# Kernel tuning notes

Hardware: AMD Instinct MI355X
Metric: run time of the kernel (lower is better)

## Reference

```python
import jax, jax.numpy as jnp
import numpy as np

N = 4096  # number of image features; must equal D because forward does attn @ img_feats.T
D = 4096


def setup_inputs() -> dict:
    key = jax.random.key(0)
    img_feats = jax.random.normal(key, (N, D), dtype=jnp.float32)
    return {"img_feats": img_feats}


def reference(img_feats):
    d = img_feats.shape[-1]
    x = img_feats / jnp.sqrt(jnp.asarray(d, img_feats.dtype))
    sims = x @ x.T  # [N, N] self-similarity
    n = sims.shape[0]
    idx = jnp.arange(n)
    sims = sims.at[idx, idx].set(-jnp.inf)  # mask self-similarity on the diagonal
    attn = jax.nn.softmax(sims, axis=-1)  # [N, N]
    return attn @ x.T  # [N, N] (requires N == D, as in the original)
```

## Files before the change

### kernel.cpp

```cpp
#include <hip/hip_runtime.h>
#include <hip/hip_bf16.h>
#include <stdint.h>

#define N 4096
#define BM 128
#define BN 128
#define BK 64
#define BK8 128

typedef __hip_bfloat16 bf16;
typedef __attribute__((ext_vector_type(8))) __bf16 bfrag;
typedef __attribute__((ext_vector_type(4))) float floatx4;
typedef __attribute__((ext_vector_type(8))) int i32x8;
typedef __attribute__((ext_vector_type(4))) int i32x4;

__device__ __forceinline__ void gld_lds16(const void* g, void* l) {
    __builtin_amdgcn_global_load_lds(
        (const __attribute__((address_space(1))) void*)g,
        (__attribute__((address_space(3))) void*)l, 16, 0, 0);
}

__device__ __forceinline__ unsigned short f2bf(float x) {
    __hip_bfloat16 h = __float2bfloat16(x);
    return *(unsigned short*)&h;
}

__global__ __launch_bounds__(256) void cvt_scale(const float* __restrict__ in,
                                                 unsigned short* __restrict__ xb,
                                                 uint8_t* __restrict__ x8,
                                                 float* __restrict__ rowsum) {
    if (blockIdx.x < 16) rowsum[blockIdx.x * 256 + threadIdx.x] = 0.f;
    const long i = ((long)blockIdx.x * 256 + threadIdx.x) * 8;
    float4 a = *(const float4*)(in + i);
    float4 b = *(const float4*)(in + i + 4);
    const float sc = 0.015625f;
    float v[8] = {a.x, a.y, a.z, a.w, b.x, b.y, b.z, b.w};
    alignas(16) unsigned short r[8];
#pragma unroll
    for (int k = 0; k < 8; ++k) r[k] = f2bf(v[k] * sc);
    *(uint4*)(xb + i) = *(const uint4*)r;

    int p0 = __builtin_amdgcn_cvt_pk_fp8_f32(v[0], v[1], 0, false);
    p0     = __builtin_amdgcn_cvt_pk_fp8_f32(v[2], v[3], p0, true);
    int p1 = __builtin_amdgcn_cvt_pk_fp8_f32(v[4], v[5], 0, false);
    p1     = __builtin_amdgcn_cvt_pk_fp8_f32(v[6], v[7], p1, true);
    int2 pk; pk.x = p0; pk.y = p1;
    *(int2*)(x8 + i) = pk;
}

__global__ __launch_bounds__(512) void gemm_sym(const uint8_t* __restrict__ X8,
                                                unsigned short* __restrict__ E,
                                                float* __restrict__ rowsum) {
    __shared__ __align__(16) char smem[32768];
    uint8_t* As = (uint8_t*)smem;
    uint8_t* Bs = (uint8_t*)(smem + 16384);

    const int t    = threadIdx.x;
    const int lane = t & 63;
    const int wave = t >> 6;
    const int wm   = wave >> 2;
    const int wn   = wave & 3;

    const int b = blockIdx.x;
    int I = (int)((sqrtf((float)(8 * b + 1)) - 1.0f) * 0.5f);
    if ((I + 1) * (I + 2) / 2 <= b) ++I;
    if (I * (I + 1) / 2 > b) --I;
    const int Jb = b - I * (I + 1) / 2;
    const int bm = I * BM;
    const int bn = Jb * BM;
    const bool diag = (I == Jb);

    floatx4 acc[4][2] = {};

    const int srow = t >> 3;
    const int skb  = (t & 7) ^ (srow & 7);
    const uint8_t* Ag = X8 + (long)(bm + srow) * N + skb * 16;
    const uint8_t* Bg = X8 + (long)(bn + srow) * N + skb * 16;
    uint8_t* Asl = As + t * 16;
    uint8_t* Bsl = Bs + t * 16;

    for (int k0 = 0; k0 < N; k0 += BK8) {
#pragma unroll
        for (int i = 0; i < 2; ++i) {
            gld_lds16(Ag + (long)i * 64 * N + k0, Asl + i * 8192);
            gld_lds16(Bg + (long)i * 64 * N + k0, Bsl + i * 8192);
        }
        __syncthreads();

        const int l15 = lane & 15;
        const int l7  = lane & 7;
        const int q   = lane >> 4;
        i32x8 af[4], bfr[2];
#pragma unroll
        for (int i = 0; i < 4; ++i) {
            const int row = wm * 64 + i * 16 + l15;
            i32x4 lo = *(const i32x4*)&As[(row * 8 + ((2 * q) ^ l7)) * 16];
            i32x4 hi = *(const i32x4*)&As[(row * 8 + ((2 * q + 1) ^ l7)) * 16];
            af[i] = (i32x8){lo.x, lo.y, lo.z, lo.w, hi.x, hi.y, hi.z, hi.w};
        }
#pragma unroll
        for (int j = 0; j < 2; ++j) {
            const int row = wn * 32 + j * 16 + l15;
            i32x4 lo = *(const i32x4*)&Bs[(row * 8 + ((2 * q) ^ l7)) * 16];
            i32x4 hi = *(const i32x4*)&Bs[(row * 8 + ((2 * q + 1) ^ l7)) * 16];
            bfr[j] = (i32x8){lo.x, lo.y, lo.z, lo.w, hi.x, hi.y, hi.z, hi.w};
        }
#pragma unroll
        for (int i = 0; i < 4; ++i)
#pragma unroll
            for (int j = 0; j < 2; ++j)
                acc[i][j] = __builtin_amdgcn_mfma_scale_f32_16x16x128_f8f6f4(
                    af[i], bfr[j], acc[i][j],
                    0, 0,
                    0, 0x79797979,
                    0, 0x79797979);
        __syncthreads();
    }

    const int l15  = lane & 15;
    const int q    = lane >> 4;
    const int col0 = bn + wn * 32 + l15;
    const int row0 = bm + wm * 64 + q * 4;

#pragma unroll
    for (int i = 0; i < 4; ++i) {
#pragma unroll
        for (int r = 0; r < 4; ++r) {
            const int row = row0 + i * 16 + r;
            float rs = 0.f;
#pragma unroll
            for (int j = 0; j < 2; ++j) {
                const int col = col0 + j * 16;
                float e = (row == col) ? 0.f : __expf(acc[i][j][r]);
                acc[i][j][r] = e;
                rs += e;
                E[(long)row * N + col] = f2bf(e);
            }
#pragma unroll
            for (int off = 1; off < 16; off <<= 1) rs += __shfl_xor(rs, off);
            if (l15 == 0) atomicAdd(rowsum + row, rs);
        }
    }

    if (!diag) {
#pragma unroll
        for (int j = 0; j < 2; ++j) {
            float cs = 0.f;
#pragma unroll
            for (int i = 0; i < 4; ++i)
#pragma unroll
                for (int r = 0; r < 4; ++r) cs += acc[i][j][r];
            cs += __shfl_xor(cs, 16);
            cs += __shfl_xor(cs, 32);
            if (q == 0) atomicAdd(rowsum + bn + wn * 32 + j * 16 + l15, cs);
        }

        unsigned short* tb = (unsigned short*)smem + wave * 2048;
        __syncthreads();
#pragma unroll
        for (int i = 0; i < 4; ++i) {
            const int lr0 = i * 16 + q * 4;
            const int blk = lr0 >> 3;
            const int half = (lr0 >> 2) & 1;
#pragma unroll
            for (int j = 0; j < 2; ++j) {
                const int lc = j * 16 + l15;
                union { unsigned short u[4]; uint2 v2; } pk;
#pragma unroll
                for (int r = 0; r < 4; ++r) pk.u[r] = f2bf(acc[i][j][r]);
                *(uint2*)&tb[lc * 64 + 8 * (blk ^ (lc & 7)) + 4 * half] = pk.v2;
            }
        }
        __syncthreads();

        const int gr0 = lane >> 3;
        const int cb  = lane & 7;
#pragma unroll
        for (int p = 0; p < 4; ++p) {
            const int gr = p * 8 + gr0;
            uint4 v = *(const uint4*)&tb[gr * 64 + 8 * (cb ^ (gr & 7))];
            *(uint4*)&E[(long)(bn + wn * 32 + gr) * N + bm + wm * 64 + cb * 8] = v;
        }
    }
}

__global__ __launch_bounds__(256) void gemm_pv(const bf16* __restrict__ A,
                                               const bf16* __restrict__ B,
                                               float* __restrict__ C,
                                               const float* __restrict__ rowsum) {
    __shared__ bf16 As[BM * BK];
    __shared__ bf16 Bs[BN * BK];

    const int t    = threadIdx.x;
    const int lane = t & 63;
    const int wave = t >> 6;
    const int wm   = wave >> 1;
    const int wn   = wave & 1;
    const int bm   = blockIdx.y * BM;
    const int bn   = blockIdx.x * BN;

    floatx4 acc[4][4] = {};

    const int srow = t >> 3;
    const int skb  = (t & 7) ^ (srow & 7);
    const bf16* Ag = A + (long)(bm + srow) * N + skb * 8;
    const bf16* Bg = B + (long)(bn + srow) * N + skb * 8;
    bf16* Asl = As + t * 8;
    bf16* Bsl = Bs + t * 8;

    for (int k0 = 0; k0 < N; k0 += BK) {
#pragma unroll
        for (int i = 0; i < 4; ++i) {
            gld_lds16(Ag + (long)i * 32 * N + k0, Asl + i * 2048);
            gld_lds16(Bg + (long)i * 32 * N + k0, Bsl + i * 2048);
        }
        __syncthreads();

        const int l15 = lane & 15;
        const int l7  = lane & 7;
        const int q   = lane >> 4;
#pragma unroll
        for (int kk = 0; kk < BK; kk += 32) {
            const int kw = (kk >> 3) + q;
            const int sw = kw ^ l7;
            bfrag a[4], b[4];
#pragma unroll
            for (int i = 0; i < 4; ++i)
                a[i] = *(const bfrag*)&As[((wm * 64 + i * 16 + l15) * 8 + sw) * 8];
#pragma unroll
            for (int j = 0; j < 4; ++j)
                b[j] = *(const bfrag*)&Bs[((wn * 64 + j * 16 + l15) * 8 + sw) * 8];
#pragma unroll
            for (int i = 0; i < 4; ++i)
#pragma unroll
                for (int j = 0; j < 4; ++j)
                    acc[i][j] = __builtin_amdgcn_mfma_f32_16x16x32_bf16(
                        a[i], b[j], acc[i][j], 0, 0, 0);
        }
        __syncthreads();
    }

    const int col0 = bn + wn * 64 + (lane & 15);
    const int row0 = bm + wm * 64 + (lane >> 4) * 4;
#pragma unroll
    for (int i = 0; i < 4; ++i) {
#pragma unroll
        for (int r = 0; r < 4; ++r) {
            const int row = row0 + i * 16 + r;
            const float inv = 1.0f / rowsum[row];
#pragma unroll
            for (int j = 0; j < 4; ++j)
                C[(long)row * N + col0 + j * 16] = acc[i][j][r] * inv;
        }
    }
}

extern "C" void kernel_launch(void* const* d_in, const int* in_sizes, int n_in,
                              void* d_out, int out_size, void* d_ws, size_t ws_size,
                              hipStream_t stream) {
    const float* in = (const float*)d_in[0];
    float* out = (float*)d_out;

    float* rowsum = (float*)d_ws;
    bf16* xb = (bf16*)((char*)d_ws + 16384);
    unsigned short* E = (unsigned short*)((char*)d_ws + 16384 + (size_t)N * N * sizeof(bf16));
    uint8_t* x8 = (uint8_t*)d_out;

    cvt_scale<<<(N * (long)N) / (256 * 8), 256, 0, stream>>>(
        in, (unsigned short*)xb, x8, rowsum);

    gemm_sym<<<528, 512, 0, stream>>>(x8, E, rowsum);
    dim3 grid(N / BN, N / BM);
    gemm_pv<<<grid, 256, 0, stream>>>((const bf16*)E, xb, out, rowsum);
}
```

Before: 316.1 us.

## Rewrite PV GEMM as 256x256 tile, 8-wave double-buffered pipelined kernel

Replaces the 128x128 single-buffered PV GEMM with a 256x256-tile kernel using 512 threads and double-buffered LDS. Global-to-LDS loads for upcoming K-slices are interleaved with MFMA sub-blocks, with explicit barriers, vmcnt/lgkmcnt waits and setprio. Block indices are swizzled for L2 locality. The aim is to hide load latency and raise arithmetic intensity, at the cost of heavy register pressure (128 accumulators per lane), 128KB of LDS per block, and fragile hand-placed synchronization.

```diff
diff --git a/kernel.cpp b/kernel.cpp
--- a/kernel.cpp
+++ b/kernel.cpp
@@ -5,8 +5,10 @@
 #define N 4096
 #define BM 128
 #define BN 128
-#define BK 64
 #define BK8 128
+#define PM 256
+#define PN 256
+#define PK 64
 
 typedef __hip_bfloat16 bf16;
 typedef __attribute__((ext_vector_type(8))) __bf16 bfrag;
@@ -184,73 +186,127 @@
     }
 }
 
-__global__ __launch_bounds__(256) void gemm_pv(const bf16* __restrict__ A,
-                                               const bf16* __restrict__ B,
-                                               float* __restrict__ C,
-                                               const float* __restrict__ rowsum) {
-    __shared__ bf16 As[BM * BK];
-    __shared__ bf16 Bs[BN * BK];
+#define PV_BAR()   __builtin_amdgcn_s_barrier()
+#define PV_LGKM0() asm volatile("s_waitcnt lgkmcnt(0)" ::: "memory")
+#define PV_VM4()   asm volatile("s_waitcnt vmcnt(4)" ::: "memory")
+
+#define PV_STAGE_A(buf, h, k0) do { \
+    const bf16* s_ = Asrc + (h) * 128 * (long)N + (k0); \
+    bf16* d_ = dstl + (buf) * 16384 + (h) * 8192; \
+    gld_lds16(s_, d_); \
+    gld_lds16(s_ + 64 * (long)N, d_ + 4096); } while (0)
+
+#define PV_STAGE_B(buf, h, k0) do { \
+    const bf16* s_ = Bsrc + (h) * 128 * (long)N + (k0); \
+    bf16* d_ = dstl + 32768 + (buf) * 16384 + (h) * 8192; \
+    gld_lds16(s_, d_); \
+    gld_lds16(s_ + 64 * (long)N, d_ + 4096); } while (0)
+
+#define PV_LDA(buf, mi) do { \
+    const bf16* b_ = lds + (buf) * 16384; \
+    _Pragma("unroll") for (int f_ = 0; f_ < 4; ++f_) { \
+      const int r_ = wm * 128 + (mi) * 64 + f_ * 16 + l15; \
+      ar[f_][0] = *(const bfrag*)&b_[(r_ * 8 + (q ^ l7)) * 8]; \
+      ar[f_][1] = *(const bfrag*)&b_[(r_ * 8 + ((4 + q) ^ l7)) * 8]; } } while (0)
+
+#define PV_LDB(buf, nj) do { \
+    const bf16* b_ = lds + 32768 + (buf) * 16384; \
+    _Pragma("unroll") for (int g_ = 0; g_ < 2; ++g_) { \
+      const int r_ = wn * 64 + (nj) * 32 + g_ * 16 + l15; \
+      br[nj][g_][0] = *(const bfrag*)&b_[(r_ * 8 + (q ^ l7)) * 8]; \
+      br[nj][g_][1] = *(const bfrag*)&b_[(r_ * 8 + ((4 + q) ^ l7)) * 8]; } } while (0)
+
+#define PV_MM(mi, nj) do { \
+    __builtin_amdgcn_s_setprio(1); \
+    _Pragma("unroll") for (int f_ = 0; f_ < 4; ++f_) \
+    _Pragma("unroll") for (int g_ = 0; g_ < 2; ++g_) \
+    _Pragma("unroll") for (int k_ = 0; k_ < 2; ++k_) \
+      acc[(mi)*4+f_][(nj)*2+g_] = __builtin_amdgcn_mfma_f32_16x16x32_bf16( \
+          ar[f_][k_], br[nj][g_][k_], acc[(mi)*4+f_][(nj)*2+g_], 0, 0, 0); \
+    __builtin_amdgcn_s_setprio(0); } while (0)
+
+__global__ __launch_bounds__(512, 2) void gemm_pv(const bf16* __restrict__ A,
+                                                  const bf16* __restrict__ B,
+                                                  float* __restrict__ C,
+                                                  const float* __restrict__ rowsum) {
+    __shared__ __align__(16) bf16 lds[4 * 16384];
 
     const int t    = threadIdx.x;
     const int lane = t & 63;
-    const int wave = t >> 6;
-    const int wm   = wave >> 1;
-    const int wn   = wave & 1;
-    const int bm   = blockIdx.y * BM;
-    const int bn   = blockIdx.x * BN;
-
-    floatx4 acc[4][4] = {};
+    const int wm   = (t >> 6) >> 2;
+    const int wn   = (t >> 6) & 3;
+    const int l15  = lane & 15;
+    const int l7   = lane & 7;
+    const int q    = lane >> 4;
+
+    const int swz = (blockIdx.x & 7) * 32 + (blockIdx.x >> 3);
+    const int bm  = (swz >> 4) * PM;
+    const int bn  = (swz & 15) * PN;
 
     const int srow = t >> 3;
     const int skb  = (t & 7) ^ (srow & 7);
-    const bf16* Ag = A + (long)(bm + srow) * N + skb * 8;
-    const bf16* Bg = B + (long)(bn + srow) * N + skb * 8;
-    bf16* Asl = As + t * 8;
-    bf16* Bsl = Bs + t * 8;
-
-    for (int k0 = 0; k0 < N; k0 += BK) {
-#pragma unroll
-        for (int i = 0; i < 4; ++i) {
-            gld_lds16(Ag + (long)i * 32 * N + k0, Asl + i * 2048);
-            gld_lds16(Bg + (long)i * 32 * N + k0, Bsl + i * 2048);
-        }
-        __syncthreads();
-
-        const int l15 = lane & 15;
-        const int l7  = lane & 7;
-        const int q   = lane >> 4;
-#pragma unroll
-        for (int kk = 0; kk < BK; kk += 32) {
-            const int kw = (kk >> 3) + q;
-            const int sw = kw ^ l7;
-            bfrag a[4], b[4];
-#pragma unroll
-            for (int i = 0; i < 4; ++i)
-                a[i] = *(const bfrag*)&As[((wm * 64 + i * 16 + l15) * 8 + sw) * 8];
-#pragma unroll
-            for (int j = 0; j < 4; ++j)
-                b[j] = *(const bfrag*)&Bs[((wn * 64 + j * 16 + l15) * 8 + sw) * 8];
-#pragma unroll
-            for (int i = 0; i < 4; ++i)
-#pragma unroll
-                for (int j = 0; j < 4; ++j)
-                    acc[i][j] = __builtin_amdgcn_mfma_f32_16x16x32_bf16(
-                        a[i], b[j], acc[i][j], 0, 0, 0);
-        }
-        __syncthreads();
-    }
-
-    const int col0 = bn + wn * 64 + (lane & 15);
-    const int row0 = bm + wm * 64 + (lane >> 4) * 4;
-#pragma unroll
-    for (int i = 0; i < 4; ++i) {
+    const bf16* Asrc = A + (long)(bm + srow) * N + skb * 8;
+    const bf16* Bsrc = B + (long)(bn + srow) * N + skb * 8;
+    bf16* dstl = lds + t * 8;
+
+    floatx4 acc[8][4] = {};
+    bfrag ar[4][2], br[2][2][2];
+
+    PV_STAGE_B(0, 0, 0); PV_STAGE_B(0, 1, 0);
+    PV_STAGE_A(0, 0, 0); PV_STAGE_A(0, 1, 0);
+    PV_STAGE_B(1, 0, PK); PV_STAGE_B(1, 1, PK);
+    PV_VM4();
+    PV_BAR();
+
+    for (int i = 0; i < 32; ++i) {
+        const int ka1 = ((2 * i + 1) * PK) & (N - 1);
+        const int kb2 = ((2 * i + 2) * PK) & (N - 1);
+        const int kb3 = ((2 * i + 3) * PK) & (N - 1);
+        PV_LDA(0, 0); PV_LDB(0, 0); PV_STAGE_A(1, 0, ka1);
+        PV_BAR(); PV_LGKM0();
+        PV_MM(0, 0);
+        PV_BAR();
+        PV_LDB(0, 1); PV_STAGE_A(1, 1, ka1);
+        PV_BAR(); PV_LGKM0();
+        PV_MM(0, 1);
+        PV_BAR();
+        PV_LDA(0, 1); PV_STAGE_B(0, 0, kb2);
+        PV_BAR(); PV_LGKM0();
+        PV_MM(1, 1);
+        PV_BAR();
+        PV_STAGE_B(0, 1, kb2);
+        PV_BAR();
+        PV_MM(1, 0);
+        PV_VM4(); PV_BAR();
+        PV_LDA(1, 0); PV_LDB(1, 0); PV_STAGE_A(0, 0, kb2);
+        PV_BAR(); PV_LGKM0();
+        PV_MM(0, 0);
+        PV_BAR();
+        PV_LDB(1, 1); PV_STAGE_A(0, 1, kb2);
+        PV_BAR(); PV_LGKM0();
+        PV_MM(0, 1);
+        PV_BAR();
+        PV_LDA(1, 1); PV_STAGE_B(1, 0, kb3);
+        PV_BAR(); PV_LGKM0();
+        PV_MM(1, 1);
+        PV_BAR();
+        PV_STAGE_B(1, 1, kb3);
+        PV_BAR();
+        PV_MM(1, 0);
+        PV_VM4(); PV_BAR();
+    }
+
+    const int rowbase = bm + wm * 128 + q * 4;
+    const int colbase = bn + wn * 64 + l15;
+#pragma unroll
+    for (int f = 0; f < 8; ++f) {
 #pragma unroll
         for (int r = 0; r < 4; ++r) {
-            const int row = row0 + i * 16 + r;
+            const int row = rowbase + f * 16 + r;
             const float inv = 1.0f / rowsum[row];
 #pragma unroll
-            for (int j = 0; j < 4; ++j)
-                C[(long)row * N + col0 + j * 16] = acc[i][j][r] * inv;
+            for (int g = 0; g < 4; ++g)
+                C[(long)row * N + colbase + g * 16] = acc[f][g][r] * inv;
         }
     }
 }
@@ -270,6 +326,5 @@
         in, (unsigned short*)xb, x8, rowsum);
 
     gemm_sym<<<528, 512, 0, stream>>>(x8, E, rowsum);
-    dim3 grid(N / BN, N / BM);
-    gemm_pv<<<grid, 256, 0, stream>>>((const bf16*)E, xb, out, rowsum);
-}
+    gemm_pv<<<256, 512, 0, stream>>>((const bf16*)E, xb, out, rowsum);
+}
```

New measurement: 285.5 us. 1.11x faster.
